# Kernel optimization log

Measured on AMD Instinct MI355X. Metric: run time of the kernel, lower is better.

The kernel has to match this reference:

```python
import jax, jax.numpy as jnp
import numpy as np

B, T, R = 128, 20, 49           # batch, caption length, num regions (7x7)
V, E, H, FD, A = 10000, 512, 512, 512, 256  # vocab, embed, hidden, feature, attn dims


def setup_inputs() -> dict:
    key = jax.random.key(0)
    ks = jax.random.split(key, 16)
    s = 0.02
    return {
        "features": jax.random.normal(ks[0], (B, R, FD), dtype=jnp.float32),
        "captions": jax.random.randint(ks[1], (B, T), 0, V),
        "emb": jax.random.normal(ks[2], (V, E), dtype=jnp.float32) * s,
        "W_h": jax.random.normal(ks[3], (A, H), dtype=jnp.float32) * s,
        "b_h": jnp.zeros((A,), jnp.float32),
        "W_f": jax.random.normal(ks[4], (A, FD), dtype=jnp.float32) * s,
        "b_f": jnp.zeros((A,), jnp.float32),
        "v_w": jax.random.normal(ks[5], (A,), dtype=jnp.float32) * s,
        "v_b": jnp.zeros((), jnp.float32),
        "W_ih": jax.random.normal(ks[6], (4 * H, E + FD), dtype=jnp.float32) * s,
        "W_hh": jax.random.normal(ks[7], (4 * H, H), dtype=jnp.float32) * s,
        "b_ih": jnp.zeros((4 * H,), jnp.float32),
        "b_hh": jnp.zeros((4 * H,), jnp.float32),
        "fc_W": jax.random.normal(ks[8], (V, H), dtype=jnp.float32) * s,
        "fc_b": jnp.zeros((V,), jnp.float32),
    }


def reference(features, captions, emb, W_h, b_h, W_f, b_f, v_w, v_b,
              W_ih, W_hh, b_ih, b_hh, fc_W, fc_b):
    Bn = features.shape[0]
    Hd = W_hh.shape[1]
    # features are constant across timesteps -> project once (same math as per-step W_f(features))
    f_proj = jnp.einsum('brf,af->bra', features, W_f) + b_f  # (B,R,A)
    embeds = emb[captions[:, :-1]]                            # (B,T-1,E)
    xs = jnp.swapaxes(embeds, 0, 1)                           # (T-1,B,E)
    bias = b_ih + b_hh

    def step(carry, x_t):
        hx, cx = carry
        # Bahdanau attention
        h = hx @ W_h.T + b_h                                  # (B,A)
        scores = jnp.tanh(h[:, None, :] + f_proj) @ v_w + v_b  # (B,R)
        alpha = jax.nn.softmax(scores, axis=1)
        context = jnp.einsum('br,brf->bf', alpha, features)   # (B,FD)
        # LSTMCell (PyTorch gate order: i,f,g,o)
        lstm_in = jnp.concatenate([x_t, context], axis=1)     # (B,E+FD)
        gates = lstm_in @ W_ih.T + hx @ W_hh.T + bias         # (B,4H)
        i, f, g, o = jnp.split(gates, 4, axis=1)
        cx = jax.nn.sigmoid(f) * cx + jax.nn.sigmoid(i) * jnp.tanh(g)
        hx = jax.nn.sigmoid(o) * jnp.tanh(cx)
        logit = hx @ fc_W.T + fc_b                            # (B,V)
        return (hx, cx), logit

    init = (jnp.zeros((Bn, Hd), features.dtype), jnp.zeros((Bn, Hd), features.dtype))
    _, logits = jax.lax.scan(step, init, xs)                  # (T-1,B,V)
    return jnp.swapaxes(logits, 0, 1)                         # (B,T-1,V)
```

## Files before the change

### kernel.cpp

```cpp
#include <hip/hip_runtime.h>
#include <hip/hip_bf16.h>
#include <math.h>

#define NB 128
#define NT 20
#define NS 19
#define NR 49
#define NV 10000
#define NE 512
#define NH 512
#define NFD 512
#define NA 256
#define NG 2048
#define NK2 1024

typedef __bf16 bf16_t;
typedef bf16_t bf16x8 __attribute__((ext_vector_type(8)));
typedef float f32x4 __attribute__((ext_vector_type(4)));

__device__ __forceinline__ float sigm(float x) { return 1.f / (1.f + expf(-x)); }

__device__ __forceinline__ void cvt8(bf16_t* d, const float* s) {
    float4 a = *(const float4*)s;
    float4 b = *(const float4*)(s + 4);
    bf16x8 v;
    v[0] = (bf16_t)a.x; v[1] = (bf16_t)a.y; v[2] = (bf16_t)a.z; v[3] = (bf16_t)a.w;
    v[4] = (bf16_t)b.x; v[5] = (bf16_t)b.y; v[6] = (bf16_t)b.z; v[7] = (bf16_t)b.w;
    *(bf16x8*)d = v;
}

__global__ __launch_bounds__(256) void k_prep(
    const float* __restrict__ fc_W, const float* __restrict__ W_ih,
    const float* __restrict__ W_hh, const float* __restrict__ W_h,
    const float* __restrict__ W_f, const float* __restrict__ features,
    const float* __restrict__ emb, const int* __restrict__ captions,
    const float* __restrict__ b_ih, const float* __restrict__ b_hh,
    const float* __restrict__ b_f, const float* __restrict__ b_h,
    bf16_t* __restrict__ fcWb, bf16_t* __restrict__ Wcat2,
    bf16_t* __restrict__ Wxg, bf16_t* __restrict__ W_hb,
    bf16_t* __restrict__ Wfb, bf16_t* __restrict__ featb,
    bf16_t* __restrict__ linx, float* __restrict__ bias,
    float* __restrict__ bfh, float* __restrict__ hx, float* __restrict__ cx)
{
    int g = blockIdx.x * 256 + threadIdx.x;
    if (g < 640000) { int idx = g * 8; cvt8(fcWb + idx, fc_W + idx); return; }
    g -= 640000;
    if (g < 262144) {
        int idx = g * 8;
        int row = idx >> 10, col = idx & 1023;
        int orig = (row & 3) * NH + (row >> 2);
        const float* src = (col < 512) ? (W_ih + (size_t)orig * 1024 + 512 + col)
                                       : (W_hh + (size_t)orig * 512 + (col - 512));
        cvt8(Wcat2 + idx, src);
        return;
    }
    g -= 262144;
    if (g < 131072) {
        int idx = g * 8;
        int row = idx >> 9, col = idx & 511;
        int orig = (row & 3) * NH + (row >> 2);
        cvt8(Wxg + idx, W_ih + (size_t)orig * 1024 + col);
        return;
    }
    g -= 131072;
    if (g < 16384) { int idx = g * 8; cvt8(W_hb + idx, W_h + idx); return; }
    g -= 16384;
    if (g < 16384) { int idx = g * 8; cvt8(Wfb + idx, W_f + idx); return; }
    g -= 16384;
    if (g < 401408) { int idx = g * 8; cvt8(featb + idx, features + idx); return; }
    g -= 401408;
    if (g < 155648) {
        int idx = g * 8;
        int row = idx >> 9, col = idx & 511;
        int t = row >> 7, b = row & 127;
        int cap = captions[b * NT + t];
        cvt8(linx + idx, emb + (size_t)cap * NE + col);
        return;
    }
    g -= 155648;
    if (g < 256) {
        int n0 = g * 8;
        #pragma unroll
        for (int i = 0; i < 8; ++i) {
            int n = n0 + i, h = n >> 2, gg = n & 3;
            int orig = gg * NH + h;
            bias[n] = b_ih[orig] + b_hh[orig];
        }
        return;
    }
    g -= 256;
    if (g < 32) {
        int n0 = g * 8;
        #pragma unroll
        for (int i = 0; i < 8; ++i) bfh[n0 + i] = b_f[n0 + i] + b_h[n0 + i];
        return;
    }
    g -= 32;
    float4 z = make_float4(0.f, 0.f, 0.f, 0.f);
    if (g < 8192) { *(float4*)(hx + g * 8) = z; *(float4*)(hx + g * 8 + 4) = z; return; }
    g -= 8192;
    if (g < 8192) { *(float4*)(cx + g * 8) = z; *(float4*)(cx + g * 8 + 4) = z; }
}

__global__ __launch_bounds__(256) void gemm_bf16_nt(
    const bf16_t* __restrict__ Am, const bf16_t* __restrict__ Bm,
    const float* __restrict__ bias, float* __restrict__ Cf,
    bf16_t* __restrict__ Cb, int M, int N, int K, int ldc)
{
    __shared__ uint4 AsU[512];
    __shared__ uint4 BsU[512];
    int tid = threadIdx.x;
    int m0 = blockIdx.x * 64, n0 = blockIdx.y * 64;
    int nk = K >> 6;

    int rowS = tid >> 3, slotS = tid & 7;
    int wr0 = rowS * 8 + (slotS ^ (rowS & 7));
    int rowS2 = rowS + 32;
    int wr1 = rowS2 * 8 + (slotS ^ (rowS2 & 7));

    const uint4* pA = (const uint4*)(Am + (size_t)(m0 + rowS) * K) + slotS;
    size_t aStep = (size_t)4 * K;
    int nrow0 = n0 + rowS, nrow1 = n0 + rowS2;
    bool bv0 = nrow0 < N, bv1 = nrow1 < N;
    const uint4* pB0 = (const uint4*)(Bm + (size_t)nrow0 * K) + slotS;
    const uint4* pB1 = (const uint4*)(Bm + (size_t)nrow1 * K) + slotS;
    uint4 zz = make_uint4(0, 0, 0, 0);

    int w = tid >> 6, lane = tid & 63;
    int wm = w >> 1, wn = w & 1;
    int lr = lane & 15, lg = lane >> 4;
    int ra[2][2], rb[2][2];
    #pragma unroll
    for (int i = 0; i < 2; ++i)
        #pragma unroll
        for (int kk = 0; kk < 2; ++kk) {
            int rA = wm * 32 + i * 16 + lr;
            int rB = wn * 32 + i * 16 + lr;
            int s = kk * 4 + lg;
            ra[i][kk] = rA * 8 + (s ^ (rA & 7));
            rb[i][kk] = rB * 8 + (s ^ (rB & 7));
        }

    f32x4 acc00 = {}, acc01 = {}, acc10 = {}, acc11 = {};
    uint4 a0 = pA[0], a1 = pA[aStep];
    uint4 b0 = bv0 ? pB0[0] : zz;
    uint4 b1 = bv1 ? pB1[0] : zz;
    pA += 8; pB0 += 8; pB1 += 8;

    #pragma unroll 1
    for (int kt = 0; kt < nk; ++kt) {
        __syncthreads();
        AsU[wr0] = a0; AsU[wr1] = a1;
        BsU[wr0] = b0; BsU[wr1] = b1;
        if (kt + 1 < nk) {
            a0 = pA[0]; a1 = pA[aStep];
            b0 = bv0 ? pB0[0] : zz;
            b1 = bv1 ? pB1[0] : zz;
            pA += 8; pB0 += 8; pB1 += 8;
        }
        __syncthreads();
        const bf16x8* Af = (const bf16x8*)AsU;
        const bf16x8* Bf = (const bf16x8*)BsU;
        #pragma unroll
        for (int kk = 0; kk < 2; ++kk) {
            bf16x8 fa0 = Af[ra[0][kk]], fa1 = Af[ra[1][kk]];
            bf16x8 fb0 = Bf[rb[0][kk]], fb1 = Bf[rb[1][kk]];
            acc00 = __builtin_amdgcn_mfma_f32_16x16x32_bf16(fa0, fb0, acc00, 0, 0, 0);
            acc01 = __builtin_amdgcn_mfma_f32_16x16x32_bf16(fa0, fb1, acc01, 0, 0, 0);
            acc10 = __builtin_amdgcn_mfma_f32_16x16x32_bf16(fa1, fb0, acc10, 0, 0, 0);
            acc11 = __builtin_amdgcn_mfma_f32_16x16x32_bf16(fa1, fb1, acc11, 0, 0, 0);
        }
    }

    f32x4 av[2][2] = {{acc00, acc01}, {acc10, acc11}};
    #pragma unroll
    for (int i = 0; i < 2; ++i) {
        int mbase = m0 + wm * 32 + i * 16 + lg * 4;
        #pragma unroll
        for (int j = 0; j < 2; ++j) {
            int n = n0 + wn * 32 + j * 16 + lr;
            if (n < N) {
                float bz = bias ? bias[n] : 0.f;
                #pragma unroll
                for (int r = 0; r < 4; ++r) {
                    float v = av[i][j][r] + bz;
                    if (Cb) Cb[(size_t)(mbase + r) * ldc + n] = (bf16_t)v;
                    else    Cf[(size_t)(mbase + r) * ldc + n] = v;
                }
            }
        }
    }
}

__global__ __launch_bounds__(512) void k_attn(
    const float* __restrict__ hx, const bf16_t* __restrict__ W_hb,
    const bf16_t* __restrict__ fprojb, const float* __restrict__ v_w,
    const bf16_t* __restrict__ featb, bf16_t* __restrict__ lin)
{
    int b = blockIdx.x;
    int tid = threadIdx.x;
    int w = tid >> 6, lane = tid & 63;
    __shared__ float hxs[NH];
    __shared__ float part[2][NA];
    __shared__ float salpha[64];

    hxs[tid] = hx[b * NH + tid];
    __syncthreads();

    {
        int a = tid & 255, q = tid >> 8;
        const bf16x8* wrow = (const bf16x8*)(W_hb + (size_t)a * NH + q * 256);
        const float* hq = hxs + q * 256;
        float p = 0.f;
        #pragma unroll
        for (int c = 0; c < 32; ++c) {
            bf16x8 wv = wrow[c];
            int k = c * 8;
            p += hq[k+0]*(float)wv[0] + hq[k+1]*(float)wv[1]
               + hq[k+2]*(float)wv[2] + hq[k+3]*(float)wv[3]
               + hq[k+4]*(float)wv[4] + hq[k+5]*(float)wv[5]
               + hq[k+6]*(float)wv[6] + hq[k+7]*(float)wv[7];
        }
        part[q][a] = p;
    }
    __syncthreads();

    {
        for (int r = w; r < NR; r += 8) {
            const bf16_t* fp = fprojb + ((size_t)b * NR + r) * NA;
            float s = 0.f;
            #pragma unroll
            for (int j = 0; j < 4; ++j) {
                int aa = lane + 64 * j;
                float hv = part[0][aa] + part[1][aa];
                s += tanhf(hv + (float)fp[aa]) * v_w[aa];
            }
            #pragma unroll
            for (int off = 32; off; off >>= 1) s += __shfl_xor(s, off);
            if (lane == 0) salpha[r] = s;
        }
    }
    __syncthreads();

    if (tid < 64) {
        float v = (tid < NR) ? salpha[tid] : -INFINITY;
        float m = v;
        #pragma unroll
        for (int off = 32; off; off >>= 1) m = fmaxf(m, __shfl_xor(m, off));
        float e = (tid < NR) ? expf(v - m) : 0.f;
        float ssum = e;
        #pragma unroll
        for (int off = 32; off; off >>= 1) ssum += __shfl_xor(ssum, off);
        if (tid < NR) salpha[tid] = e / ssum;
    }
    __syncthreads();

    {
        bf16_t* lrow = lin + (size_t)b * NK2;
        float c = 0.f;
        #pragma unroll 7
        for (int r = 0; r < NR; ++r)
            c += salpha[r] * (float)featb[((size_t)b * NR + r) * NFD + tid];
        lrow[tid] = (bf16_t)c;
        lrow[NFD + tid] = (bf16_t)hxs[tid];
    }
}

__global__ __launch_bounds__(256) void k_step(
    const bf16_t* __restrict__ lin, const bf16_t* __restrict__ Wcat2,
    const bf16_t* __restrict__ pre_x, const float* __restrict__ bias,
    float* __restrict__ hx, float* __restrict__ cx,
    bf16_t* __restrict__ hxAll, int t)
{
    __shared__ __align__(16) char smem[12288];
    uint4* AsU = (uint4*)smem;
    uint4* BsU = AsU + 256;

    int tid = threadIdx.x;
    int m0 = blockIdx.x * 32, n0 = blockIdx.y * 64;

    int rowS = tid >> 3, slotS = tid & 7;
    int wrA = rowS * 8 + (slotS ^ (rowS & 7));
    int rowB2 = rowS + 32;
    int wrB1 = rowB2 * 8 + (slotS ^ (rowB2 & 7));

    const uint4* pA  = (const uint4*)(lin   + (size_t)(m0 + rowS) * NK2) + slotS;
    const uint4* pB0 = (const uint4*)(Wcat2 + (size_t)(n0 + rowS) * NK2) + slotS;
    const uint4* pB1 = (const uint4*)(Wcat2 + (size_t)(n0 + rowB2) * NK2) + slotS;

    int w = tid >> 6, lane = tid & 63;
    int wm = w & 1, wn = w >> 1;
    int lr = lane & 15, lg = lane >> 4;
    int raI[2], rbI[2][2];
    #pragma unroll
    for (int kk = 0; kk < 2; ++kk) {
        int rA = wm * 16 + lr;
        int s = kk * 4 + lg;
        raI[kk] = rA * 8 + (s ^ (rA & 7));
        #pragma unroll
        for (int j = 0; j < 2; ++j) {
            int rB = wn * 32 + j * 16 + lr;
            rbI[j][kk] = rB * 8 + (s ^ (rB & 7));
        }
    }

    f32x4 acc0 = {}, acc1 = {};
    uint4 a0 = pA[0], b0 = pB0[0], b1 = pB1[0];
    pA += 8; pB0 += 8; pB1 += 8;

    #pragma unroll 1
    for (int kt = 0; kt < NK2 / 64; ++kt) {
        __syncthreads();
        AsU[wrA] = a0; BsU[wrA] = b0; BsU[wrB1] = b1;
        if (kt + 1 < NK2 / 64) {
            a0 = pA[0]; b0 = pB0[0]; b1 = pB1[0];
            pA += 8; pB0 += 8; pB1 += 8;
        }
        __syncthreads();
        const bf16x8* Af = (const bf16x8*)AsU;
        const bf16x8* Bf = (const bf16x8*)BsU;
        #pragma unroll
        for (int kk = 0; kk < 2; ++kk) {
            bf16x8 fa  = Af[raI[kk]];
            bf16x8 fb0 = Bf[rbI[0][kk]];
            bf16x8 fb1 = Bf[rbI[1][kk]];
            acc0 = __builtin_amdgcn_mfma_f32_16x16x32_bf16(fa, fb0, acc0, 0, 0, 0);
            acc1 = __builtin_amdgcn_mfma_f32_16x16x32_bf16(fa, fb1, acc1, 0, 0, 0);
        }
    }

    __syncthreads();
    float* Ct = (float*)smem;
    {
        int crow = wm * 16 + lg * 4;
        #pragma unroll
        for (int r = 0; r < 4; ++r) {
            Ct[(crow + r) * 65 + wn * 32 + lr]      = acc0[r];
            Ct[(crow + r) * 65 + wn * 32 + 16 + lr] = acc1[r];
        }
    }
    __syncthreads();

    int hloc = tid & 15;
    int h = (n0 >> 2) + hloc;
    #pragma unroll
    for (int q = 0; q < 2; ++q) {
        int m = (tid >> 4) + q * 16;
        int bb = m0 + m;
        const float* crow = Ct + m * 65 + hloc * 4;
        const float* brow = bias + n0 + hloc * 4;
        const bf16_t* prow = pre_x + ((size_t)t * NB + bb) * NG + n0 + hloc * 4;
        float gi = crow[0] + brow[0] + (float)prow[0];
        float gf = crow[1] + brow[1] + (float)prow[1];
        float gg = crow[2] + brow[2] + (float)prow[2];
        float go = crow[3] + brow[3] + (float)prow[3];
        size_t idx = (size_t)bb * NH + h;
        float c = sigm(gf) * cx[idx] + sigm(gi) * tanhf(gg);
        float hn = sigm(go) * tanhf(c);
        cx[idx] = c;
        hx[idx] = hn;
        hxAll[((size_t)t * NB + bb) * NH + h] = (bf16_t)hn;
    }
}

__global__ __launch_bounds__(256) void k_logits(
    const bf16_t* __restrict__ hxAll, const bf16_t* __restrict__ fcWb,
    const float* __restrict__ fc_b, float* __restrict__ out)
{
    __shared__ uint4 AsU[512];
    __shared__ uint4 BsU[512];
    int tid = threadIdx.x;
    int m0 = blockIdx.x * 64, n0 = blockIdx.y * 64;

    int rowS = tid >> 3, slotS = tid & 7;
    int wr0 = rowS * 8 + (slotS ^ (rowS & 7));
    int rowS2 = rowS + 32;
    int wr1 = rowS2 * 8 + (slotS ^ (rowS2 & 7));

    const uint4* pA = (const uint4*)(hxAll + (size_t)(m0 + rowS) * NH) + slotS;
    size_t aStep = (size_t)4 * NH;
    int nrow0 = n0 + rowS, nrow1 = n0 + rowS2;
    bool bv0 = nrow0 < NV, bv1 = nrow1 < NV;
    const uint4* pB0 = (const uint4*)(fcWb + (size_t)nrow0 * NH) + slotS;
    const uint4* pB1 = (const uint4*)(fcWb + (size_t)nrow1 * NH) + slotS;
    uint4 zz = make_uint4(0, 0, 0, 0);

    int w = tid >> 6, lane = tid & 63;
    int wm = w >> 1, wn = w & 1;
    int lr = lane & 15, lg = lane >> 4;
    int ra[2][2], rb[2][2];
    #pragma unroll
    for (int i = 0; i < 2; ++i)
        #pragma unroll
        for (int kk = 0; kk < 2; ++kk) {
            int rA = wm * 32 + i * 16 + lr;
            int rB = wn * 32 + i * 16 + lr;
            int s = kk * 4 + lg;
            ra[i][kk] = rA * 8 + (s ^ (rA & 7));
            rb[i][kk] = rB * 8 + (s ^ (rB & 7));
        }

    f32x4 acc00 = {}, acc01 = {}, acc10 = {}, acc11 = {};
    uint4 a0 = pA[0], a1 = pA[aStep];
    uint4 b0 = bv0 ? pB0[0] : zz;
    uint4 b1 = bv1 ? pB1[0] : zz;
    pA += 8; pB0 += 8; pB1 += 8;

    #pragma unroll 1
    for (int kt = 0; kt < NH / 64; ++kt) {
        __syncthreads();
        AsU[wr0] = a0; AsU[wr1] = a1;
        BsU[wr0] = b0; BsU[wr1] = b1;
        if (kt + 1 < NH / 64) {
            a0 = pA[0]; a1 = pA[aStep];
            b0 = bv0 ? pB0[0] : zz;
            b1 = bv1 ? pB1[0] : zz;
            pA += 8; pB0 += 8; pB1 += 8;
        }
        __syncthreads();
        const bf16x8* Af = (const bf16x8*)AsU;
        const bf16x8* Bf = (const bf16x8*)BsU;
        #pragma unroll
        for (int kk = 0; kk < 2; ++kk) {
            bf16x8 fa0 = Af[ra[0][kk]], fa1 = Af[ra[1][kk]];
            bf16x8 fb0 = Bf[rb[0][kk]], fb1 = Bf[rb[1][kk]];
            acc00 = __builtin_amdgcn_mfma_f32_16x16x32_bf16(fa0, fb0, acc00, 0, 0, 0);
            acc01 = __builtin_amdgcn_mfma_f32_16x16x32_bf16(fa0, fb1, acc01, 0, 0, 0);
            acc10 = __builtin_amdgcn_mfma_f32_16x16x32_bf16(fa1, fb0, acc10, 0, 0, 0);
            acc11 = __builtin_amdgcn_mfma_f32_16x16x32_bf16(fa1, fb1, acc11, 0, 0, 0);
        }
    }

    f32x4 av[2][2] = {{acc00, acc01}, {acc10, acc11}};
    #pragma unroll
    for (int i = 0; i < 2; ++i) {
        int mbase = m0 + wm * 32 + i * 16 + lg * 4;
        #pragma unroll
        for (int j = 0; j < 2; ++j) {
            int n = n0 + wn * 32 + j * 16 + lr;
            if (n < NV) {
                float bz = fc_b[n];
                #pragma unroll
                for (int r = 0; r < 4; ++r) {
                    int m = mbase + r;
                    int bb = m & 127, tt = m >> 7;
                    __builtin_nontemporal_store(
                        av[i][j][r] + bz,
                        out + ((size_t)bb * NS + tt) * NV + n);
                }
            }
        }
    }
}

extern "C" void kernel_launch(void* const* d_in, const int* in_sizes, int n_in,
                              void* d_out, int out_size, void* d_ws, size_t ws_size,
                              hipStream_t stream)
{
    const float* features = (const float*)d_in[0];
    const int*   captions = (const int*)d_in[1];
    const float* emb      = (const float*)d_in[2];
    const float* W_h      = (const float*)d_in[3];
    const float* b_h      = (const float*)d_in[4];
    const float* W_f      = (const float*)d_in[5];
    const float* b_f      = (const float*)d_in[6];
    const float* v_w      = (const float*)d_in[7];
    const float* W_ih     = (const float*)d_in[9];
    const float* W_hh     = (const float*)d_in[10];
    const float* b_ih     = (const float*)d_in[11];
    const float* b_hh     = (const float*)d_in[12];
    const float* fc_W     = (const float*)d_in[13];
    const float* fc_b     = (const float*)d_in[14];
    float* out = (float*)d_out;

    char* base = (char*)d_ws;
    bf16_t* fcWb   = (bf16_t*)base;  base += (size_t)NV * NH * 2;
    bf16_t* Wcat2  = (bf16_t*)base;  base += (size_t)NG * NK2 * 2;
    bf16_t* Wxg    = (bf16_t*)base;  base += (size_t)NG * NE * 2;
    bf16_t* W_hb   = (bf16_t*)base;  base += (size_t)NA * NH * 2;
    bf16_t* Wfb    = (bf16_t*)base;  base += (size_t)NA * NFD * 2;
    bf16_t* featb  = (bf16_t*)base;  base += (size_t)NB * NR * NFD * 2;
    bf16_t* linx   = (bf16_t*)base;  base += (size_t)NS * NB * NE * 2;
    bf16_t* pre_x  = (bf16_t*)base;  base += (size_t)NS * NB * NG * 2;
    bf16_t* lin    = (bf16_t*)base;  base += (size_t)NB * NK2 * 2;
    bf16_t* hxAll  = (bf16_t*)base;  base += (size_t)NS * NB * NH * 2;
    bf16_t* fprojb = (bf16_t*)base;  base += (size_t)NB * NR * NA * 2;
    float*  bias   = (float*)base;   base += (size_t)NG * 4;
    float*  bfh    = (float*)base;   base += (size_t)NA * 4;
    float*  hx     = (float*)base;   base += (size_t)NB * NH * 4;
    float*  cx     = (float*)base;   base += (size_t)NB * NH * 4;

    k_prep<<<dim3(6406), 256, 0, stream>>>(
        fc_W, W_ih, W_hh, W_h, W_f, features, emb, captions, b_ih, b_hh,
        b_f, b_h, fcWb, Wcat2, Wxg, W_hb, Wfb, featb, linx, bias, bfh, hx, cx);

    gemm_bf16_nt<<<dim3(98, 4), 256, 0, stream>>>(
        featb, Wfb, bfh, (float*)0, fprojb, NB * NR, NA, NFD, NA);

    gemm_bf16_nt<<<dim3(38, 32), 256, 0, stream>>>(
        linx, Wxg, (const float*)0, (float*)0, pre_x, NS * NB, NG, NE, NG);

    for (int t = 0; t < NS; ++t) {
        k_attn<<<dim3(NB), 512, 0, stream>>>(
            hx, W_hb, fprojb, v_w, featb, lin);
        k_step<<<dim3(4, 32), 256, 0, stream>>>(
            lin, Wcat2, pre_x, bias, hx, cx, hxAll, t);
    }

    k_logits<<<dim3(38, 157), 256, 0, stream>>>(hxAll, fcWb, fc_b, out);
}
```

Before: 670.3 us.

## Fuse next-step attention into LSTM step kernel via per-batch-tile counter barrier

Merges the per-step attention kernel into the LSTM step kernel, which removes one launch per timestep. After the gate update, the 32 blocks sharing a batch tile synchronise on an atomic counter that is spin-waited in global memory. Each block then computes attention and the context vector for one batch row, for use in the next step. The spin-wait assumes all 32 blocks in a group are resident at once (the grid is 128 blocks), and it adds atomic and fence overhead and a serialized wait inside the kernel.

```diff
diff --git a/kernel.cpp b/kernel.cpp
--- a/kernel.cpp
+++ b/kernel.cpp
@@ -40,7 +40,8 @@
     bf16_t* __restrict__ Wxg, bf16_t* __restrict__ W_hb,
     bf16_t* __restrict__ Wfb, bf16_t* __restrict__ featb,
     bf16_t* __restrict__ linx, float* __restrict__ bias,
-    float* __restrict__ bfh, float* __restrict__ hx, float* __restrict__ cx)
+    float* __restrict__ bfh, float* __restrict__ hx, float* __restrict__ cx,
+    unsigned* __restrict__ cnt)
 {
     int g = blockIdx.x * 256 + threadIdx.x;
     if (g < 640000) { int idx = g * 8; cvt8(fcWb + idx, fc_W + idx); return; }
@@ -99,7 +100,12 @@
     float4 z = make_float4(0.f, 0.f, 0.f, 0.f);
     if (g < 8192) { *(float4*)(hx + g * 8) = z; *(float4*)(hx + g * 8 + 4) = z; return; }
     g -= 8192;
-    if (g < 8192) { *(float4*)(cx + g * 8) = z; *(float4*)(cx + g * 8 + 4) = z; }
+    if (g < 8192) { *(float4*)(cx + g * 8) = z; *(float4*)(cx + g * 8 + 4) = z; return; }
+    g -= 8192;
+    if (g < 16) {
+        #pragma unroll
+        for (int i = 0; i < 8; ++i) cnt[g * 8 + i] = 0u;
+    }
 }
 
 __global__ __launch_bounds__(256) void gemm_bf16_nt(
@@ -266,11 +272,14 @@
     }
 }
 
-__global__ __launch_bounds__(256) void k_step(
-    const bf16_t* __restrict__ lin, const bf16_t* __restrict__ Wcat2,
-    const bf16_t* __restrict__ pre_x, const float* __restrict__ bias,
-    float* __restrict__ hx, float* __restrict__ cx,
-    bf16_t* __restrict__ hxAll, int t)
+__global__ __launch_bounds__(256) void k_fused(
+    bf16_t* lin,
+    const bf16_t* __restrict__ Wcat2, const bf16_t* __restrict__ pre_x,
+    const float* __restrict__ bias, float* __restrict__ hx,
+    float* __restrict__ cx, bf16_t* __restrict__ hxAll,
+    const bf16_t* __restrict__ W_hb, const bf16_t* __restrict__ fprojb,
+    const float* __restrict__ v_w, const bf16_t* __restrict__ featb,
+    unsigned* cnt, int t, int last)
 {
     __shared__ __align__(16) char smem[12288];
     uint4* AsU = (uint4*)smem;
@@ -341,25 +350,109 @@
     }
     __syncthreads();
 
-    int hloc = tid & 15;
-    int h = (n0 >> 2) + hloc;
-    #pragma unroll
-    for (int q = 0; q < 2; ++q) {
-        int m = (tid >> 4) + q * 16;
-        int bb = m0 + m;
-        const float* crow = Ct + m * 65 + hloc * 4;
-        const float* brow = bias + n0 + hloc * 4;
-        const bf16_t* prow = pre_x + ((size_t)t * NB + bb) * NG + n0 + hloc * 4;
-        float gi = crow[0] + brow[0] + (float)prow[0];
-        float gf = crow[1] + brow[1] + (float)prow[1];
-        float gg = crow[2] + brow[2] + (float)prow[2];
-        float go = crow[3] + brow[3] + (float)prow[3];
-        size_t idx = (size_t)bb * NH + h;
-        float c = sigm(gf) * cx[idx] + sigm(gi) * tanhf(gg);
-        float hn = sigm(go) * tanhf(c);
-        cx[idx] = c;
-        hx[idx] = hn;
-        hxAll[((size_t)t * NB + bb) * NH + h] = (bf16_t)hn;
+    {
+        int hloc = tid & 15;
+        int h = (n0 >> 2) + hloc;
+        #pragma unroll
+        for (int q = 0; q < 2; ++q) {
+            int m = (tid >> 4) + q * 16;
+            int bb = m0 + m;
+            const float* crow = Ct + m * 65 + hloc * 4;
+            const float* brow = bias + n0 + hloc * 4;
+            const bf16_t* prow = pre_x + ((size_t)t * NB + bb) * NG + n0 + hloc * 4;
+            float gi = crow[0] + brow[0] + (float)prow[0];
+            float gf = crow[1] + brow[1] + (float)prow[1];
+            float gg = crow[2] + brow[2] + (float)prow[2];
+            float go = crow[3] + brow[3] + (float)prow[3];
+            size_t idx = (size_t)bb * NH + h;
+            float c = sigm(gf) * cx[idx] + sigm(gi) * tanhf(gg);
+            float hn = sigm(go) * tanhf(c);
+            cx[idx] = c;
+            hx[idx] = hn;
+            hxAll[((size_t)t * NB + bb) * NH + h] = (bf16_t)hn;
+        }
+    }
+    if (last) return;
+
+    __syncthreads();
+    unsigned* flag = cnt + t * 4 + blockIdx.x;
+    if (tid == 0) {
+        __threadfence();
+        atomicAdd(flag, 1u);
+        while (__hip_atomic_load(flag, __ATOMIC_RELAXED, __HIP_MEMORY_SCOPE_AGENT) < 32u)
+            __builtin_amdgcn_s_sleep(2);
+    }
+    __syncthreads();
+    __threadfence();
+
+    int bb = m0 + blockIdx.y;
+    float* hxs  = (float*)smem;
+    float* hatt = hxs + NH;
+    float* salp = hatt + NA;
+
+    hxs[tid]       = hx[(size_t)bb * NH + tid];
+    hxs[tid + 256] = hx[(size_t)bb * NH + tid + 256];
+    __syncthreads();
+
+    {
+        const bf16x8* wrow = (const bf16x8*)(W_hb + (size_t)tid * NH);
+        float p = 0.f;
+        #pragma unroll
+        for (int c = 0; c < 64; ++c) {
+            bf16x8 wv = wrow[c];
+            int k = c * 8;
+            p += hxs[k+0]*(float)wv[0] + hxs[k+1]*(float)wv[1]
+               + hxs[k+2]*(float)wv[2] + hxs[k+3]*(float)wv[3]
+               + hxs[k+4]*(float)wv[4] + hxs[k+5]*(float)wv[5]
+               + hxs[k+6]*(float)wv[6] + hxs[k+7]*(float)wv[7];
+        }
+        hatt[tid] = p;
+    }
+    __syncthreads();
+
+    {
+        for (int r = w; r < NR; r += 4) {
+            const bf16_t* fp = fprojb + ((size_t)bb * NR + r) * NA;
+            float s = 0.f;
+            #pragma unroll
+            for (int jj = 0; jj < 4; ++jj) {
+                int aa = lane + 64 * jj;
+                s += tanhf(hatt[aa] + (float)fp[aa]) * v_w[aa];
+            }
+            #pragma unroll
+            for (int off = 32; off; off >>= 1) s += __shfl_xor(s, off);
+            if (lane == 0) salp[r] = s;
+        }
+    }
+    __syncthreads();
+
+    if (tid < 64) {
+        float v = (tid < NR) ? salp[tid] : -INFINITY;
+        float m = v;
+        #pragma unroll
+        for (int off = 32; off; off >>= 1) m = fmaxf(m, __shfl_xor(m, off));
+        float e = (tid < NR) ? expf(v - m) : 0.f;
+        float ssum = e;
+        #pragma unroll
+        for (int off = 32; off; off >>= 1) ssum += __shfl_xor(ssum, off);
+        if (tid < NR) salp[tid] = e / ssum;
+    }
+    __syncthreads();
+
+    {
+        bf16_t* lrow = lin + (size_t)bb * NK2;
+        float c0 = 0.f, c1 = 0.f;
+        #pragma unroll 7
+        for (int r = 0; r < NR; ++r) {
+            const bf16_t* fr = featb + ((size_t)bb * NR + r) * NFD;
+            float al = salp[r];
+            c0 += al * (float)fr[tid];
+            c1 += al * (float)fr[tid + 256];
+        }
+        lrow[tid]             = (bf16_t)c0;
+        lrow[tid + 256]       = (bf16_t)c1;
+        lrow[NFD + tid]       = (bf16_t)hxs[tid];
+        lrow[NFD + tid + 256] = (bf16_t)hxs[tid + 256];
     }
 }
 
@@ -489,10 +582,12 @@
     float*  bfh    = (float*)base;   base += (size_t)NA * 4;
     float*  hx     = (float*)base;   base += (size_t)NB * NH * 4;
     float*  cx     = (float*)base;   base += (size_t)NB * NH * 4;
+    unsigned* cnt  = (unsigned*)base; base += 128 * 4;
 
     k_prep<<<dim3(6406), 256, 0, stream>>>(
         fc_W, W_ih, W_hh, W_h, W_f, features, emb, captions, b_ih, b_hh,
-        b_f, b_h, fcWb, Wcat2, Wxg, W_hb, Wfb, featb, linx, bias, bfh, hx, cx);
+        b_f, b_h, fcWb, Wcat2, Wxg, W_hb, Wfb, featb, linx, bias, bfh,
+        hx, cx, cnt);
 
     gemm_bf16_nt<<<dim3(98, 4), 256, 0, stream>>>(
         featb, Wfb, bfh, (float*)0, fprojb, NB * NR, NA, NFD, NA);
@@ -500,11 +595,12 @@
     gemm_bf16_nt<<<dim3(38, 32), 256, 0, stream>>>(
         linx, Wxg, (const float*)0, (float*)0, pre_x, NS * NB, NG, NE, NG);
 
+    k_attn<<<dim3(NB), 512, 0, stream>>>(hx, W_hb, fprojb, v_w, featb, lin);
+
     for (int t = 0; t < NS; ++t) {
-        k_attn<<<dim3(NB), 512, 0, stream>>>(
-            hx, W_hb, fprojb, v_w, featb, lin);
-        k_step<<<dim3(4, 32), 256, 0, stream>>>(
-            lin, Wcat2, pre_x, bias, hx, cx, hxAll, t);
+        k_fused<<<dim3(4, 32), 256, 0, stream>>>(
+            lin, Wcat2, pre_x, bias, hx, cx, hxAll,
+            W_hb, fprojb, v_w, featb, cnt, t, (t == NS - 1) ? 1 : 0);
     }
 
     k_logits<<<dim3(38, 157), 256, 0, stream>>>(hxAll, fcWb, fc_b, out);
```

Result: slower. 1.050 ms (+56.7%).
